# Performance work log

Hardware: AMD Instinct MI355X
Metric: run time of the kernel (lower is better)

## Reference

```python
import jax, jax.numpy as jnp
import numpy as np
import math

B, LA, LB, H = 64, 512, 512, 768


def setup_inputs() -> dict:
    key = jax.random.key(0)
    k1, k2 = jax.random.split(key)
    a = jax.random.normal(k1, (B, LA, H), dtype=jnp.float32)
    b = jax.random.normal(k2, (B, LB, H), dtype=jnp.float32)
    mask_a = jnp.ones((B, LA, 1), dtype=jnp.int32)
    mask_b = jnp.ones((B, LB, 1), dtype=jnp.int32)
    temperature = jnp.asarray(1.0 / math.sqrt(H), dtype=jnp.float32)
    return {"a": a, "b": b, "mask_a": mask_a, "mask_b": mask_b,
            "temperature": temperature}


def reference(a, b, mask_a, mask_b, temperature):
    # attn[b, i, j] = <a_i, b_j> * temperature   -> [B, LA, LB]
    attn = jnp.einsum('bih,bjh->bij', a, b) * temperature
    # pair mask: valid where both positions valid
    mask = jnp.einsum('bik,bjk->bij', mask_a.astype(jnp.float32),
                      mask_b.astype(jnp.float32)) > 0
    NEG = jnp.float32(-1e7)
    attn = jnp.where(mask, attn, NEG)
    attn_a = jax.nn.softmax(attn, axis=1)  # softmax over LA (columns normalize)
    attn_b = jax.nn.softmax(attn, axis=2)  # softmax over LB (rows normalize)
    feature_b = jnp.einsum('bij,bih->bjh', attn_a, a)  # [B, LB, H]
    feature_a = jnp.einsum('bij,bjh->bih', attn_b, b)  # [B, LA, H]
    return feature_a, feature_b
```

## Files before the change

kernel.cpp:

```cpp
#include <hip/hip_runtime.h>
#include <stdint.h>

typedef _Float16 f16;
typedef _Float16 half8_t __attribute__((ext_vector_type(8)));
typedef _Float16 half4_t __attribute__((ext_vector_type(4)));
typedef float floatx4 __attribute__((ext_vector_type(4)));

#define B_  64
#define LA_ 512
#define LB_ 512
#define H_  768

static __device__ __forceinline__ int swz(int row, int byteInRow) {
    return row * 128 + (byteInRow ^ ((row & 7) << 4));
}

static __device__ __forceinline__ void gload16(const void* g, void* l) {
    __builtin_amdgcn_global_load_lds(
        (const __attribute__((address_space(1))) unsigned int*)g,
        (__attribute__((address_space(3))) unsigned int*)l,
        16, 0, 0);
}

__global__ __launch_bounds__(256) void conv_kernel(
    const float* __restrict__ A, const float* __restrict__ Bm,
    f16* __restrict__ a16, f16* __restrict__ b16,
    f16* __restrict__ aT, f16* __restrict__ bT)
{
    __shared__ f16 Ts[64][68];

    const int t  = threadIdx.x;
    const int hb = blockIdx.x * 64, lb = blockIdx.y * 64;
    const int z  = blockIdx.z, b = z >> 1, which = z & 1;

    const float* src = which ? Bm : A;
    f16* d  = which ? b16 : a16;
    f16* dT = which ? bT : aT;

    const int r = t >> 2, cs = (t & 3) * 16;
    const float* s = src + (size_t)(b * 512 + lb + r) * H_ + hb + cs;

    f16 hv[16];
    #pragma unroll
    for (int q = 0; q < 4; ++q) {
        floatx4 v = ((const floatx4*)s)[q];
        #pragma unroll
        for (int e = 0; e < 4; ++e) hv[q * 4 + e] = (f16)v[e];
    }

    f16* drow = d + (size_t)(b * 512 + lb + r) * H_ + hb + cs;
    {
        half8_t u0, u1;
        #pragma unroll
        for (int e = 0; e < 8; ++e) { u0[e] = hv[e]; u1[e] = hv[8 + e]; }
        *(half8_t*)drow = u0;
        *(half8_t*)(drow + 8) = u1;
    }

    #pragma unroll
    for (int e = 0; e < 16; ++e) Ts[r][cs + e] = hv[e];
    __syncthreads();

    const int h = t >> 2, ls = (t & 3) * 16;
    half8_t v0, v1;
    #pragma unroll
    for (int e = 0; e < 8; ++e) { v0[e] = Ts[ls + e][h]; v1[e] = Ts[ls + 8 + e][h]; }
    f16* dTrow = dT + ((size_t)b * H_ + hb + h) * 512 + lb + ls;
    *(half8_t*)dTrow = v0;
    *(half8_t*)(dTrow + 8) = v1;
}

__global__ __launch_bounds__(256) void qk16_kernel(
    const f16* __restrict__ A16, const f16* __restrict__ B16,
    const int* __restrict__ maskA, const int* __restrict__ maskB,
    const float* __restrict__ temp_p,
    f16* __restrict__ P, f16* __restrict__ PT)
{
    __shared__ f16 As[2][128 * 64];
    __shared__ f16 Bs[2][128 * 64];
    __shared__ int mA[128];
    __shared__ int mB[128];

    const int t    = threadIdx.x;
    const int lane = t & 63;
    const int w    = t >> 6;
    const int wm   = w >> 1, wn = w & 1;

    int id = (int)blockIdx.x;
    id = (id & 7) * 128 + (id >> 3);
    const int jb = (id & 3) * 128;
    const int ib = ((id >> 2) & 3) * 128;
    const int b  = id >> 4;

    if (t < 128)      mA[t]       = maskA[b * LA_ + ib + t];
    else              mB[t - 128] = maskB[b * LB_ + jb + (t - 128)];

    floatx4 acc[4][4] = {};

    const f16* Ab = A16 + (size_t)(b * LA_ + ib) * H_;
    const f16* Bb = B16 + (size_t)(b * LB_ + jb) * H_;

    int srow[4], sbyt[4];
    #pragma unroll
    for (int q = 0; q < 4; ++q) {
        const int o = (q * 4 + w) * 1024 + lane * 16;
        srow[q] = o >> 7;
        sbyt[q] = (o & 127) ^ ((srow[q] & 7) << 4);
    }

    #define QK_STAGE(bufi, kt)                                            \
        _Pragma("unroll")                                                 \
        for (int q = 0; q < 4; ++q) {                                     \
            const int wc = q * 4 + w;                                     \
            const size_t go = (size_t)srow[q] * H_ + (kt) * 64 + (sbyt[q] >> 1); \
            gload16(Ab + go, (char*)As[bufi] + wc * 1024);                \
            gload16(Bb + go, (char*)Bs[bufi] + wc * 1024);                \
        }

    QK_STAGE(0, 0);
    int cur = 0;

    for (int kt = 0; kt < H_ / 64; ++kt) {
        __syncthreads();
        if (kt + 1 < H_ / 64) { QK_STAGE(cur ^ 1, kt + 1); }

        char* AsB = (char*)As[cur];
        char* BsB = (char*)Bs[cur];
        #pragma unroll
        for (int ks = 0; ks < 2; ++ks) {
            half8_t af[4], bf[4];
            #pragma unroll
            for (int m = 0; m < 4; ++m) {
                const int r = wm * 64 + m * 16 + (lane & 15);
                af[m] = *(half8_t*)(AsB + swz(r, ks * 64 + ((lane >> 4) << 4)));
            }
            #pragma unroll
            for (int n = 0; n < 4; ++n) {
                const int r = wn * 64 + n * 16 + (lane & 15);
                bf[n] = *(half8_t*)(BsB + swz(r, ks * 64 + ((lane >> 4) << 4)));
            }
            #pragma unroll
            for (int m = 0; m < 4; ++m)
                #pragma unroll
                for (int n = 0; n < 4; ++n)
                    acc[m][n] = __builtin_amdgcn_mfma_f32_16x16x32_f16(
                        af[m], bf[n], acc[m][n], 0, 0, 0);
        }
        cur ^= 1;
    }
    #undef QK_STAGE

    const float temp = *temp_p;
    #pragma unroll
    for (int m = 0; m < 4; ++m) {
        const int iloc0 = wm * 64 + m * 16 + ((lane >> 4) << 2);
        #pragma unroll
        for (int n = 0; n < 4; ++n) {
            const int jloc = wn * 64 + n * 16 + (lane & 15);
            const int vb = mB[jloc];
            half4_t hv;
            #pragma unroll
            for (int r = 0; r < 4; ++r) {
                const int iloc = iloc0 + r;
                const float s = acc[m][n][r] * temp;
                const float p = (mA[iloc] && vb) ? __expf(s) : 0.0f;
                hv[r] = (f16)p;
                P[(size_t)(b * LA_ + ib + iloc) * LB_ + jb + jloc] = hv[r];
            }
            *(half4_t*)(PT + (size_t)(b * LB_ + jb + jloc) * LA_ + ib + iloc0) = hv;
        }
    }
}

__global__ __launch_bounds__(256) void rowsum_kernel(
    const f16* __restrict__ P, const f16* __restrict__ PT,
    float* __restrict__ lrow, float* __restrict__ lcol)
{
    const int dir = blockIdx.z;
    const f16* src = dir ? PT : P;
    float*     dst = dir ? lcol : lrow;
    const int b  = blockIdx.y;
    const int rb = blockIdx.x * 64;
    const int wv = threadIdx.x >> 6, lane = threadIdx.x & 63;

    for (int r = wv; r < 64; r += 4) {
        const int row = rb + r;
        const half8_t raw = *(const half8_t*)(src + (size_t)(b * 512 + row) * 512 + lane * 8);
        float s = 0.f;
        #pragma unroll
        for (int e = 0; e < 8; ++e) s += (float)raw[e];
        #pragma unroll
        for (int off = 32; off > 0; off >>= 1) s += __shfl_down(s, off);
        if (lane == 0) dst[b * 512 + row] = s;
    }
}

__global__ __launch_bounds__(256) void pv16_kernel(
    const f16* __restrict__ P, const f16* __restrict__ PT,
    const f16* __restrict__ aT, const f16* __restrict__ bT,
    const float* __restrict__ lrow, const float* __restrict__ lcol,
    float* __restrict__ out)
{
    __shared__ f16 As[2][128 * 64];
    __shared__ f16 Vs[2][128 * 64];
    __shared__ float Sc[128];

    const int t    = threadIdx.x;
    const int lane = t & 63;
    const int w    = t >> 6;
    const int wm   = w >> 1, wn = w & 1;

    int id = (int)blockIdx.x;
    id = (id & 7) * 384 + (id >> 3);
    const int hb = (id % 6) * 128;
    const int rem = id / 6;
    const int ib = (rem & 3) * 128;
    const int z  = rem >> 2;
    const int dir = z >> 6;
    const int b   = z & 63;

    const f16* Ab = (dir ? PT : P) + (size_t)(b * 512 + ib) * 512;
    const f16* Vb = (dir ? aT : bT) + ((size_t)b * H_ + hb) * 512;
    const float* lsrc = dir ? lcol : lrow;
    float* o = out + (size_t)dir * ((size_t)B_ * LA_ * H_)
                   + (size_t)(b * 512 + ib) * H_ + hb;

    if (t < 128) {
        const float l = lsrc[b * 512 + ib + t];
        Sc[t] = (l > 0.f) ? 1.0f / l : 0.0f;
    }

    floatx4 acc[4][4] = {};

    int srow[4], sbyt[4];
    #pragma unroll
    for (int q = 0; q < 4; ++q) {
        const int o2 = (q * 4 + w) * 1024 + lane * 16;
        srow[q] = o2 >> 7;
        sbyt[q] = (o2 & 127) ^ ((srow[q] & 7) << 4);
    }

    #define PV_STAGE(bufi, kt)                                            \
        _Pragma("unroll")                                                 \
        for (int q = 0; q < 4; ++q) {                                     \
            const int wc = q * 4 + w;                                     \
            const size_t go = (size_t)srow[q] * 512 + (kt) * 64 + (sbyt[q] >> 1); \
            gload16(Ab + go, (char*)As[bufi] + wc * 1024);                \
            gload16(Vb + go, (char*)Vs[bufi] + wc * 1024);                \
        }

    PV_STAGE(0, 0);
    int cur = 0;

    for (int kt = 0; kt < 512 / 64; ++kt) {
        __syncthreads();
        if (kt + 1 < 512 / 64) { PV_STAGE(cur ^ 1, kt + 1); }

        char* AsB = (char*)As[cur];
        char* VsB = (char*)Vs[cur];
        #pragma unroll
        for (int ks = 0; ks < 2; ++ks) {
            half8_t af[4], vf[4];
            #pragma unroll
            for (int m = 0; m < 4; ++m) {
                const int r = wm * 64 + m * 16 + (lane & 15);
                af[m] = *(half8_t*)(AsB + swz(r, ks * 64 + ((lane >> 4) << 4)));
            }
            #pragma unroll
            for (int n = 0; n < 4; ++n) {
                const int r = wn * 64 + n * 16 + (lane & 15);
                vf[n] = *(half8_t*)(VsB + swz(r, ks * 64 + ((lane >> 4) << 4)));
            }
            #pragma unroll
            for (int m = 0; m < 4; ++m)
                #pragma unroll
                for (int n = 0; n < 4; ++n)
                    acc[m][n] = __builtin_amdgcn_mfma_f32_16x16x32_f16(
                        af[m], vf[n], acc[m][n], 0, 0, 0);
        }
        cur ^= 1;
    }
    #undef PV_STAGE

    #pragma unroll
    for (int m = 0; m < 4; ++m) {
        const int iloc0 = wm * 64 + m * 16 + ((lane >> 4) << 2);
        #pragma unroll
        for (int n = 0; n < 4; ++n) {
            const int hloc = wn * 64 + n * 16 + (lane & 15);
            #pragma unroll
            for (int r = 0; r < 4; ++r) {
                const int iloc = iloc0 + r;
                o[(size_t)iloc * H_ + hloc] = acc[m][n][r] * Sc[iloc];
            }
        }
    }
}

extern "C" void kernel_launch(void* const* d_in, const int* in_sizes, int n_in,
                              void* d_out, int out_size, void* d_ws, size_t ws_size,
                              hipStream_t stream)
{
    const float* a    = (const float*)d_in[0];
    const float* b    = (const float*)d_in[1];
    const int*   ma   = (const int*)d_in[2];
    const int*   mb   = (const int*)d_in[3];
    const float* temp = (const float*)d_in[4];
    float*       out  = (float*)d_out;
    char*        ws   = (char*)d_ws;

    const size_t NEW_NEED = 268697600;
    if (ws_size < NEW_NEED) return;

    f16*   a16  = (f16*)(ws);
    f16*   b16  = (f16*)(ws + 50331648);
    f16*   aT   = (f16*)(ws + 100663296);
    f16*   bT   = (f16*)(ws + 150994944);
    f16*   P    = (f16*)(ws + 201326592);
    f16*   PT   = (f16*)(ws + 234881024);
    float* lrow = (float*)(ws + 268435456);
    float* lcol = (float*)(ws + 268566528);

    conv_kernel<<<dim3(H_ / 64, 512 / 64, 2 * B_), 256, 0, stream>>>(
        a, b, a16, b16, aT, bT);
    qk16_kernel<<<dim3(1024, 1, 1), 256, 0, stream>>>(
        a16, b16, ma, mb, temp, P, PT);
    rowsum_kernel<<<dim3(512 / 64, B_, 2), 256, 0, stream>>>(P, PT, lrow, lcol);
    pv16_kernel<<<dim3(3072, 1, 1), 256, 0, stream>>>(
        P, PT, aT, bT, lrow, lcol, out);
}
```

Measured before the change: 532.4 us.

## Fuse fp32-to-fp16 conversion into QK GEMM and fold row/col sums into epilogue

The QK kernel now reads fp32 inputs directly, converting them to fp16 in registers and writing them to swizzled LDS. This removes the separate a16/b16 copies that the conversion kernel used to write and QK then re-read. Row and column sums of the exponentiated scores are accumulated in the QK epilogue via shuffles and shared/global atomics, which eliminates the rowsum kernel that re-read P and PT. In exchange, fp32 global reads double QK's input traffic, the loads are staged through registers instead of async LDS loads, and a small zero-init kernel plus global atomics are added.

Result: slower. 576.0 us (+8.2%).

```diff
diff --git a/kernel.cpp b/kernel.cpp
--- a/kernel.cpp
+++ b/kernel.cpp
@@ -22,9 +22,13 @@
         16, 0, 0);
 }
 
+__global__ __launch_bounds__(256) void zeroinit_kernel(float* __restrict__ p) {
+    const int i = blockIdx.x * 256 + threadIdx.x;
+    ((floatx4*)p)[i] = floatx4{0.f, 0.f, 0.f, 0.f};
+}
+
 __global__ __launch_bounds__(256) void conv_kernel(
     const float* __restrict__ A, const float* __restrict__ Bm,
-    f16* __restrict__ a16, f16* __restrict__ b16,
     f16* __restrict__ aT, f16* __restrict__ bT)
 {
     __shared__ f16 Ts[64][68];
@@ -34,31 +38,17 @@
     const int z  = blockIdx.z, b = z >> 1, which = z & 1;
 
     const float* src = which ? Bm : A;
-    f16* d  = which ? b16 : a16;
     f16* dT = which ? bT : aT;
 
     const int r = t >> 2, cs = (t & 3) * 16;
     const float* s = src + (size_t)(b * 512 + lb + r) * H_ + hb + cs;
 
-    f16 hv[16];
     #pragma unroll
     for (int q = 0; q < 4; ++q) {
         floatx4 v = ((const floatx4*)s)[q];
         #pragma unroll
-        for (int e = 0; e < 4; ++e) hv[q * 4 + e] = (f16)v[e];
-    }
-
-    f16* drow = d + (size_t)(b * 512 + lb + r) * H_ + hb + cs;
-    {
-        half8_t u0, u1;
-        #pragma unroll
-        for (int e = 0; e < 8; ++e) { u0[e] = hv[e]; u1[e] = hv[8 + e]; }
-        *(half8_t*)drow = u0;
-        *(half8_t*)(drow + 8) = u1;
-    }
-
-    #pragma unroll
-    for (int e = 0; e < 16; ++e) Ts[r][cs + e] = hv[e];
+        for (int e = 0; e < 4; ++e) Ts[r][cs + q * 4 + e] = (f16)v[e];
+    }
     __syncthreads();
 
     const int h = t >> 2, ls = (t & 3) * 16;
@@ -70,16 +60,19 @@
     *(half8_t*)(dTrow + 8) = v1;
 }
 
-__global__ __launch_bounds__(256) void qk16_kernel(
-    const f16* __restrict__ A16, const f16* __restrict__ B16,
+__global__ __launch_bounds__(256) void qk_f32_kernel(
+    const float* __restrict__ Ag, const float* __restrict__ Bg,
     const int* __restrict__ maskA, const int* __restrict__ maskB,
     const float* __restrict__ temp_p,
-    f16* __restrict__ P, f16* __restrict__ PT)
+    f16* __restrict__ P, f16* __restrict__ PT,
+    float* __restrict__ lrow, float* __restrict__ lcol)
 {
     __shared__ f16 As[2][128 * 64];
     __shared__ f16 Bs[2][128 * 64];
     __shared__ int mA[128];
     __shared__ int mB[128];
+    __shared__ float rsum[128];
+    __shared__ float csum[128];
 
     const int t    = threadIdx.x;
     const int lane = t & 63;
@@ -92,38 +85,45 @@
     const int ib = ((id >> 2) & 3) * 128;
     const int b  = id >> 4;
 
-    if (t < 128)      mA[t]       = maskA[b * LA_ + ib + t];
-    else              mB[t - 128] = maskB[b * LB_ + jb + (t - 128)];
+    if (t < 128) { mA[t] = maskA[b * LA_ + ib + t]; rsum[t] = 0.f; csum[t] = 0.f; }
+    else         { mB[t - 128] = maskB[b * LB_ + jb + (t - 128)]; }
 
     floatx4 acc[4][4] = {};
 
-    const f16* Ab = A16 + (size_t)(b * LA_ + ib) * H_;
-    const f16* Bb = B16 + (size_t)(b * LB_ + jb) * H_;
-
-    int srow[4], sbyt[4];
-    #pragma unroll
-    for (int q = 0; q < 4; ++q) {
-        const int o = (q * 4 + w) * 1024 + lane * 16;
-        srow[q] = o >> 7;
-        sbyt[q] = (o & 127) ^ ((srow[q] & 7) << 4);
-    }
-
-    #define QK_STAGE(bufi, kt)                                            \
+    const int row  = t >> 1;
+    const int half = t & 1;
+    const float* srcA = Ag + (size_t)(b * LA_ + ib + row) * H_ + half * 32;
+    const float* srcB = Bg + (size_t)(b * LB_ + jb + row) * H_ + half * 32;
+
+    floatx4 a4[8], b4[8];
+    #define QK_LOAD(kt)                                                   \
+        {                                                                 \
+            const floatx4* pa = (const floatx4*)(srcA + (kt) * 64);       \
+            const floatx4* pb = (const floatx4*)(srcB + (kt) * 64);       \
+            _Pragma("unroll")                                             \
+            for (int q = 0; q < 8; ++q) { a4[q] = pa[q]; b4[q] = pb[q]; } \
+        }
+    #define QK_DSWRITE(bufi)                                              \
         _Pragma("unroll")                                                 \
         for (int q = 0; q < 4; ++q) {                                     \
-            const int wc = q * 4 + w;                                     \
-            const size_t go = (size_t)srow[q] * H_ + (kt) * 64 + (sbyt[q] >> 1); \
-            gload16(Ab + go, (char*)As[bufi] + wc * 1024);                \
-            gload16(Bb + go, (char*)Bs[bufi] + wc * 1024);                \
-        }
-
-    QK_STAGE(0, 0);
+            half8_t ha, hb;                                               \
+            _Pragma("unroll")                                             \
+            for (int e = 0; e < 8; ++e) {                                 \
+                ha[e] = (f16)(a4[2 * q + (e >> 2)][e & 3]);               \
+                hb[e] = (f16)(b4[2 * q + (e >> 2)][e & 3]);               \
+            }                                                             \
+            const int off = swz(row, (half * 4 + q) * 16);                \
+            *(half8_t*)((char*)As[bufi] + off) = ha;                      \
+            *(half8_t*)((char*)Bs[bufi] + off) = hb;                      \
+        }
+
+    QK_LOAD(0);
+    QK_DSWRITE(0);
     int cur = 0;
 
     for (int kt = 0; kt < H_ / 64; ++kt) {
+        if (kt + 1 < H_ / 64) { QK_LOAD(kt + 1); }
         __syncthreads();
-        if (kt + 1 < H_ / 64) { QK_STAGE(cur ^ 1, kt + 1); }
-
         char* AsB = (char*)As[cur];
         char* BsB = (char*)Bs[cur];
         #pragma unroll
@@ -146,11 +146,22 @@
                     acc[m][n] = __builtin_amdgcn_mfma_f32_16x16x32_f16(
                         af[m], bf[n], acc[m][n], 0, 0, 0);
         }
+        if (kt + 1 < H_ / 64) { QK_DSWRITE(cur ^ 1); }
         cur ^= 1;
     }
-    #undef QK_STAGE
+    #undef QK_LOAD
+    #undef QK_DSWRITE
 
     const float temp = *temp_p;
+    float rs[4][4];
+    float cspart[4];
+    #pragma unroll
+    for (int m = 0; m < 4; ++m)
+        #pragma unroll
+        for (int r = 0; r < 4; ++r) rs[m][r] = 0.f;
+    #pragma unroll
+    for (int n = 0; n < 4; ++n) cspart[n] = 0.f;
+
     #pragma unroll
     for (int m = 0; m < 4; ++m) {
         const int iloc0 = wm * 64 + m * 16 + ((lane >> 4) << 2);
@@ -165,34 +176,35 @@
                 const float s = acc[m][n][r] * temp;
                 const float p = (mA[iloc] && vb) ? __expf(s) : 0.0f;
                 hv[r] = (f16)p;
+                const float pf = (float)hv[r];
+                rs[m][r] += pf;
+                cspart[n] += pf;
                 P[(size_t)(b * LA_ + ib + iloc) * LB_ + jb + jloc] = hv[r];
             }
             *(half4_t*)(PT + (size_t)(b * LB_ + jb + jloc) * LA_ + ib + iloc0) = hv;
         }
     }
-}
-
-__global__ __launch_bounds__(256) void rowsum_kernel(
-    const f16* __restrict__ P, const f16* __restrict__ PT,
-    float* __restrict__ lrow, float* __restrict__ lcol)
-{
-    const int dir = blockIdx.z;
-    const f16* src = dir ? PT : P;
-    float*     dst = dir ? lcol : lrow;
-    const int b  = blockIdx.y;
-    const int rb = blockIdx.x * 64;
-    const int wv = threadIdx.x >> 6, lane = threadIdx.x & 63;
-
-    for (int r = wv; r < 64; r += 4) {
-        const int row = rb + r;
-        const half8_t raw = *(const half8_t*)(src + (size_t)(b * 512 + row) * 512 + lane * 8);
-        float s = 0.f;
-        #pragma unroll
-        for (int e = 0; e < 8; ++e) s += (float)raw[e];
-        #pragma unroll
-        for (int off = 32; off > 0; off >>= 1) s += __shfl_down(s, off);
-        if (lane == 0) dst[b * 512 + row] = s;
-    }
+
+    #pragma unroll
+    for (int m = 0; m < 4; ++m) {
+        const int iloc0 = wm * 64 + m * 16 + ((lane >> 4) << 2);
+        #pragma unroll
+        for (int r = 0; r < 4; ++r) {
+            float v = rs[m][r];
+            v += __shfl_xor(v, 1); v += __shfl_xor(v, 2);
+            v += __shfl_xor(v, 4); v += __shfl_xor(v, 8);
+            if ((lane & 15) == 0) atomicAdd(&rsum[iloc0 + r], v);
+        }
+    }
+    #pragma unroll
+    for (int n = 0; n < 4; ++n) {
+        float v = cspart[n];
+        v += __shfl_xor(v, 16); v += __shfl_xor(v, 32);
+        if (lane < 16) atomicAdd(&csum[wn * 64 + n * 16 + lane], v);
+    }
+    __syncthreads();
+    if (t < 128) atomicAdd(&lrow[b * 512 + ib + t], rsum[t]);
+    else         atomicAdd(&lcol[b * 512 + jb + (t - 128)], csum[t - 128]);
 }
 
 __global__ __launch_bounds__(256) void pv16_kernel(
@@ -309,23 +321,21 @@
     float*       out  = (float*)d_out;
     char*        ws   = (char*)d_ws;
 
-    const size_t NEW_NEED = 268697600;
-    if (ws_size < NEW_NEED) return;
-
-    f16*   a16  = (f16*)(ws);
-    f16*   b16  = (f16*)(ws + 50331648);
-    f16*   aT   = (f16*)(ws + 100663296);
-    f16*   bT   = (f16*)(ws + 150994944);
-    f16*   P    = (f16*)(ws + 201326592);
-    f16*   PT   = (f16*)(ws + 234881024);
-    float* lrow = (float*)(ws + 268435456);
-    float* lcol = (float*)(ws + 268566528);
-
+    const size_t NEED = 168034304;
+    if (ws_size < NEED) return;
+
+    f16*   aT   = (f16*)(ws);
+    f16*   bT   = (f16*)(ws + 50331648);
+    f16*   P    = (f16*)(ws + 100663296);
+    f16*   PT   = (f16*)(ws + 134217728);
+    float* lrow = (float*)(ws + 167772160);
+    float* lcol = (float*)(ws + 167903232);
+
+    zeroinit_kernel<<<dim3(64, 1, 1), 256, 0, stream>>>(lrow);
     conv_kernel<<<dim3(H_ / 64, 512 / 64, 2 * B_), 256, 0, stream>>>(
-        a, b, a16, b16, aT, bT);
-    qk16_kernel<<<dim3(1024, 1, 1), 256, 0, stream>>>(
-        a16, b16, ma, mb, temp, P, PT);
-    rowsum_kernel<<<dim3(512 / 64, B_, 2), 256, 0, stream>>>(P, PT, lrow, lcol);
+        a, b, aT, bT);
+    qk_f32_kernel<<<dim3(1024, 1, 1), 256, 0, stream>>>(
+        a, b, ma, mb, temp, P, PT, lrow, lcol);
     pv16_kernel<<<dim3(3072, 1, 1), 256, 0, stream>>>(
         P, PT, aT, bT, lrow, lcol, out);
 }
```
